# Kernel tuning notes

Measured on AMD Instinct MI355X. Metric: run time of the kernel, lower is better.

The kernel has to match this reference:

```python
import jax, jax.numpy as jnp
import numpy as np

N_M, N_C, D, H, E, EL = 200000, 50000, 128, 64, 1000000, 100000


def gat_conv(h_src, h_dst, W_src, W_dst, a_src, a_dst, b, src, dst, n_dst):
    # PyG GATConv (heads=1): project, per-edge attention logit, segment softmax over dst, weighted scatter-sum.
    hs = h_src @ W_src                      # [Ns, H]
    hd = h_dst @ W_dst                      # [Nd, H]
    al_s = hs @ a_src                       # [Ns]
    al_d = hd @ a_dst                       # [Nd]
    alpha = jax.nn.leaky_relu(al_s[src] + al_d[dst], 0.2)   # [E]
    m = jax.ops.segment_max(alpha, dst, num_segments=n_dst)
    m = jnp.where(jnp.isfinite(m), m, 0.0)
    e = jnp.exp(alpha - m[dst])
    denom = jax.ops.segment_sum(e, dst, num_segments=n_dst)
    w = e / jnp.maximum(denom[dst], 1e-16)
    out = jax.ops.segment_sum(w[:, None] * hs[src], dst, num_segments=n_dst)
    return out + b


def setup_inputs() -> dict:
    key = jax.random.key(0)
    ks = jax.random.split(key, 32)
    p = lambda k, s: (jax.random.normal(k, s, jnp.float32) * 0.1)
    inp = {
        'x_m': jax.random.normal(ks[0], (N_M, D), jnp.float32),
        'x_c': jax.random.normal(ks[1], (N_C, D), jnp.float32),
        'src_mc': jax.random.randint(ks[2], (E,), 0, N_M, jnp.int32),
        'dst_mc': jax.random.randint(ks[3], (E,), 0, N_C, jnp.int32),
        'src_cm': jax.random.randint(ks[4], (E,), 0, N_C, jnp.int32),
        'dst_cm': jax.random.randint(ks[5], (E,), 0, N_M, jnp.int32),
        'row': jax.random.randint(ks[6], (EL,), 0, N_M, jnp.int32),
        'col': jax.random.randint(ks[7], (EL,), 0, N_C, jnp.int32),
        'W1s_mc': p(ks[8], (D, H)), 'W1d_mc': p(ks[9], (D, H)),
        'a1s_mc': p(ks[10], (H,)), 'a1d_mc': p(ks[11], (H,)), 'b1_mc': p(ks[12], (H,)),
        'W1s_cm': p(ks[13], (D, H)), 'W1d_cm': p(ks[14], (D, H)),
        'a1s_cm': p(ks[15], (H,)), 'a1d_cm': p(ks[16], (H,)), 'b1_cm': p(ks[17], (H,)),
        'W2s_mc': p(ks[18], (H, H)), 'W2d_mc': p(ks[19], (H, H)),
        'a2s_mc': p(ks[20], (H,)), 'a2d_mc': p(ks[21], (H,)), 'b2_mc': p(ks[22], (H,)),
        'W2s_cm': p(ks[23], (H, H)), 'W2d_cm': p(ks[24], (H, H)),
        'a2s_cm': p(ks[25], (H,)), 'a2d_cm': p(ks[26], (H,)), 'b2_cm': p(ks[27], (H,)),
        'Wd1': p(ks[28], (2 * H, H)), 'bd1': p(ks[29], (H,)),
        'Wd2': p(ks[30], (H, 2)), 'bd2': p(ks[31], (2,)),
    }
    return inp


def reference(x_m, x_c, src_mc, dst_mc, src_cm, dst_cm, row, col,
              W1s_mc, W1d_mc, a1s_mc, a1d_mc, b1_mc,
              W1s_cm, W1d_cm, a1s_cm, a1d_cm, b1_cm,
              W2s_mc, W2d_mc, a2s_mc, a2d_mc, b2_mc,
              W2s_cm, W2d_cm, a2s_cm, a2d_cm, b2_cm,
              Wd1, bd1, Wd2, bd2):
    # Layer 1: materials receive only via concepts->materials edges; concepts via materials->concepts.
    z_c = jax.nn.relu(gat_conv(x_m, x_c, W1s_mc, W1d_mc, a1s_mc, a1d_mc, b1_mc, src_mc, dst_mc, N_C))
    z_m = jax.nn.relu(gat_conv(x_c, x_m, W1s_cm, W1d_cm, a1s_cm, a1d_cm, b1_cm, src_cm, dst_cm, N_M))
    # Layer 2 (no activation)
    z_c2 = gat_conv(z_m, z_c, W2s_mc, W2d_mc, a2s_mc, a2d_mc, b2_mc, src_mc, dst_mc, N_C)
    z_m2 = gat_conv(z_c, z_m, W2s_cm, W2d_cm, a2s_cm, a2d_cm, b2_cm, src_cm, dst_cm, N_M)
    # Edge decoder: gather-concat + 2-layer MLP (no activation between, per source)
    z = jnp.concatenate([z_m2[row], z_c2[col]], axis=-1)   # [EL, 2H]
    z = z @ Wd1 + bd1
    z = z @ Wd2 + bd2
    return z.reshape(-1)
```

## Files before the change

kernel.cpp:

```cpp
#include <hip/hip_runtime.h>
#include <hip/hip_fp16.h>
#include <cstdint>
#include <cstddef>

typedef _Float16 f16x8 __attribute__((ext_vector_type(8)));
typedef float f32x4 __attribute__((ext_vector_type(4)));

__device__ __forceinline__ float exp_am8(float a) {
    return __builtin_amdgcn_exp2f(fmaf(a, 1.442695040888963f, -11.541560327111707f));
}

__global__ __launch_bounds__(256) void bucket_hist(const int* __restrict__ dA,
                                                   int* __restrict__ bcntA, int shA,
                                                   const int* __restrict__ dB,
                                                   int* __restrict__ bcntB, int shB,
                                                   int E, int nblkA) {
    __shared__ int h[256];
    const int* dst; int* bcnt; int sh; int base;
    if ((int)blockIdx.x < nblkA) { dst = dA; bcnt = bcntA; sh = shA; base = blockIdx.x * 4096; }
    else { dst = dB; bcnt = bcntB; sh = shB; base = (blockIdx.x - nblkA) * 4096; }
    int t = threadIdx.x;
    h[t] = 0;
    __syncthreads();
#pragma unroll
    for (int j = 0; j < 16; ++j) {
        int i = base + j * 256 + t;
        if (i < E) atomicAdd(&h[dst[i] >> sh], 1);
    }
    __syncthreads();
    int c = h[t];
    if (c > 0) atomicAdd(&bcnt[t], c);
}

__global__ void bucket_scan(const int* __restrict__ bcntA, int nbkA,
                            int* __restrict__ bbaseA, int* __restrict__ bcurA,
                            int* __restrict__ offA, int nA,
                            const int* __restrict__ bcntB, int nbkB,
                            int* __restrict__ bbaseB, int* __restrict__ bcurB,
                            int* __restrict__ offB, int nB, int E) {
    int t = threadIdx.x;
    if (t == 0) {
        int run = 0;
        for (int i = 0; i < nbkA; ++i) { bbaseA[i] = run; bcurA[i] = run; run += bcntA[i]; }
        bbaseA[nbkA] = run;
        offA[nA] = E;
    }
    if (t == 64) {
        int run = 0;
        for (int i = 0; i < nbkB; ++i) { bbaseB[i] = run; bcurB[i] = run; run += bcntB[i]; }
        bbaseB[nbkB] = run;
        offB[nB] = E;
    }
}

__global__ __launch_bounds__(256) void bucket_scatter(
    const int* __restrict__ srcA, const int* __restrict__ dstA,
    int* __restrict__ bcurA, unsigned* __restrict__ pairsA,
    const int* __restrict__ srcB, const int* __restrict__ dstB,
    int* __restrict__ bcurB, unsigned* __restrict__ pairsB,
    int E, int nblkA, int shA, int shB, int srcbits) {
    __shared__ int bcnt[256];
    __shared__ int bbase[256];
    const int* src; const int* dst; int* bcur; unsigned* pairs; int sh; int base;
    if ((int)blockIdx.x < nblkA) {
        src = srcA; dst = dstA; bcur = bcurA; pairs = pairsA; sh = shA;
        base = blockIdx.x * 4096;
    } else {
        src = srcB; dst = dstB; bcur = bcurB; pairs = pairsB; sh = shB;
        base = (blockIdx.x - nblkA) * 4096;
    }
    int t = threadIdx.x;
    int msk = (1 << sh) - 1;
    bcnt[t] = 0;
    __syncthreads();
    int sreg[16], dreg[16];
#pragma unroll
    for (int j = 0; j < 16; ++j) {
        int i = base + j * 256 + t;
        if (i < E) {
            sreg[j] = src[i];
            dreg[j] = dst[i];
            atomicAdd(&bcnt[dreg[j] >> sh], 1);
        } else {
            dreg[j] = -1;
        }
    }
    __syncthreads();
    {
        int c = bcnt[t];
        int g = (c > 0) ? atomicAdd(&bcur[t], c) : 0;
        bbase[t] = g;
        bcnt[t] = 0;
    }
    __syncthreads();
#pragma unroll
    for (int j = 0; j < 16; ++j) {
        if (dreg[j] >= 0) {
            int b = dreg[j] >> sh;
            int r = atomicAdd(&bcnt[b], 1);
            pairs[bbase[b] + r] = ((unsigned)(dreg[j] & msk) << srcbits) | (unsigned)sreg[j];
        }
    }
}

__global__ __launch_bounds__(256) void bucket_expand2(
    const unsigned* __restrict__ pairsA, const int* __restrict__ bbaseA, int nA,
    int* __restrict__ offA, int* __restrict__ csrA, int shA, int nbA,
    const unsigned* __restrict__ pairsB, const int* __restrict__ bbaseB, int nB,
    int* __restrict__ offB, int* __restrict__ csrB, int shB, int srcbits) {
    __shared__ int lcnt[1024];
    __shared__ int red[256];
    const unsigned* pairs; const int* bbase; int n; int* off; int* csr; int sh; int b;
    if ((int)blockIdx.x < nbA) {
        pairs = pairsA; bbase = bbaseA; n = nA; off = offA; csr = csrA; sh = shA;
        b = blockIdx.x;
    } else {
        pairs = pairsB; bbase = bbaseB; n = nB; off = offB; csr = csrB; sh = shB;
        b = blockIdx.x - nbA;
    }
    int dpb = 1 << sh;
    int d0 = b << sh;
    int t = threadIdx.x;
    unsigned smask = (1u << srcbits) - 1u;
    for (int dl = t; dl < dpb; dl += 256) lcnt[dl] = 0;
    __syncthreads();
    int pbeg = bbase[b], pend = bbase[b + 1];
    for (int i = pbeg + t; i < pend; i += 256)
        atomicAdd(&lcnt[pairs[i] >> srcbits], 1);
    __syncthreads();
    int per = (dpb + 255) >> 8;
    int i0 = t * per;
    int s = 0;
    for (int j = 0; j < per; ++j) {
        int dl = i0 + j;
        if (dl < dpb) s += lcnt[dl];
    }
    red[t] = s;
    __syncthreads();
    for (int st = 1; st < 256; st <<= 1) {
        int tmp = (t >= st) ? red[t - st] : 0;
        __syncthreads();
        red[t] += tmp;
        __syncthreads();
    }
    int run = pbeg + red[t] - s;
    for (int j = 0; j < per; ++j) {
        int dl = i0 + j;
        if (dl < dpb) {
            int c = lcnt[dl];
            if (d0 + dl < n) off[d0 + dl] = run;
            lcnt[dl] = run;
            run += c;
        }
    }
    __syncthreads();
    for (int i = pbeg + t; i < pend; i += 256) {
        unsigned p = pairs[i];
        int dl = (int)(p >> srcbits);
        int pos = atomicAdd(&lcnt[dl], 1);
        csr[pos] = (int)(p & smask);
    }
}

__global__ __launch_bounds__(256) void pack_w_all(
    const float* __restrict__ Wa0, const float* __restrict__ Wb0, _Float16* __restrict__ P0,
    const float* __restrict__ Wa1, const float* __restrict__ Wb1, _Float16* __restrict__ P1,
    const float* __restrict__ Wa2, const float* __restrict__ Wb2, _Float16* __restrict__ P2,
    const float* __restrict__ Wa3, const float* __restrict__ Wb3, _Float16* __restrict__ P3) {
    int b = blockIdx.x;
    const float* Wa; const float* Wb; _Float16* Wp; int K; int lb;
    if (b < 64)       { Wa = Wa0; Wb = Wb0; Wp = P0; K = 128; lb = b; }
    else if (b < 128) { Wa = Wa1; Wb = Wb1; Wp = P1; K = 128; lb = b - 64; }
    else if (b < 160) { Wa = Wa2; Wb = Wb2; Wp = P2; K = 64;  lb = b - 128; }
    else              { Wa = Wa3; Wb = Wb3; Wp = P3; K = 64;  lb = b - 160; }
    int NKB = K / 32;
    int i = lb * 256 + threadIdx.x;
    if (i >= 128 * K) return;
    int k = i >> 7, c = i & 127;
    float v = (c < 64) ? Wa[k * 64 + c] : Wb[k * 64 + (c - 64)];
    int ct = c >> 4, lr = c & 15, kb = k >> 5, lk = (k & 31) >> 3, e = k & 7;
    Wp[((ct * NKB + kb) * 64 + (lr + 16 * lk)) * 8 + e] = (_Float16)v;
}

__global__ void decoder_prep2(const float* __restrict__ Wd1, const float* __restrict__ bd1,
                              const float* __restrict__ Wd2, const float* __restrict__ bd2,
                              const float* __restrict__ b2_cm, const float* __restrict__ b2_mc,
                              float* __restrict__ Wc, float* __restrict__ bc,
                              float* __restrict__ bq) {
    __shared__ float WcS[256];
    int t = threadIdx.x;
    int k = t >> 1, c = t & 1;
    float s = 0.f;
    for (int j = 0; j < 64; ++j) s += Wd1[k * 64 + j] * Wd2[j * 2 + c];
    Wc[k * 2 + c] = s;
    WcS[k * 2 + c] = s;
    if (k == 0) {
        float b = bd2[c];
        for (int j = 0; j < 64; ++j) b += bd1[j] * Wd2[j * 2 + c];
        bc[c] = b;
    }
    __syncthreads();
    if (t < 2) {
        float v = 0.f;
        for (int j = 0; j < 64; ++j) v += b2_cm[j] * WcS[j * 2 + t];
        bq[t] = v;
    } else if (t < 4) {
        int cc = t - 2;
        float v = 0.f;
        for (int j = 0; j < 64; ++j) v += b2_mc[j] * WcS[(64 + j) * 2 + cc];
        bq[t] = v;
    }
}

template <int K, typename TIN, int QMODE>
__global__ __launch_bounds__(256) void proj_mfma4_kernel(const TIN* __restrict__ X, int N,
                                                         const _Float16* __restrict__ Wp,
                                                         const float* __restrict__ a0v,
                                                         const float* __restrict__ a1v,
                                                         __half* __restrict__ out0,
                                                         const float* __restrict__ wcq,
                                                         float2* __restrict__ qtab,
                                                         float* __restrict__ al0,
                                                         float* __restrict__ al1) {
    constexpr int NKB = K / 32;
    __shared__ __align__(16) _Float16 Wlds[128 * K];
    int t = threadIdx.x;
    constexpr int NV = (128 * K) / 8;
#pragma unroll
    for (int i = t; i < NV; i += 256)
        ((uint4*)Wlds)[i] = ((const uint4*)Wp)[i];
    __syncthreads();

    int rt = blockIdx.x * 64;
    int wv = t >> 6, lane = t & 63, lr = lane & 15, lk = lane >> 4;
    int row = rt + wv * 16 + lr;
    int rowc = row < N ? row : N - 1;

    f32x4 acc[8];
#pragma unroll
    for (int i = 0; i < 8; ++i) acc[i] = f32x4{0.f, 0.f, 0.f, 0.f};

    const f16x8* Wf = (const f16x8*)Wlds;
#pragma unroll
    for (int kb = 0; kb < NKB; ++kb) {
        f16x8 bf;
        if constexpr (sizeof(TIN) == 4) {
            const float* xr = (const float*)X + (size_t)rowc * K + kb * 32 + lk * 8;
            float4 x0 = *(const float4*)xr;
            float4 x1 = *(const float4*)(xr + 4);
            bf[0] = (_Float16)x0.x; bf[1] = (_Float16)x0.y;
            bf[2] = (_Float16)x0.z; bf[3] = (_Float16)x0.w;
            bf[4] = (_Float16)x1.x; bf[5] = (_Float16)x1.y;
            bf[6] = (_Float16)x1.z; bf[7] = (_Float16)x1.w;
        } else {
            bf = *(const f16x8*)((const _Float16*)X + (size_t)rowc * K + kb * 32 + lk * 8);
        }
#pragma unroll
        for (int ct = 0; ct < 8; ++ct) {
            acc[ct] = __builtin_amdgcn_mfma_f32_16x16x32_f16(Wf[(ct * NKB + kb) * 64 + lane],
                                                             bf, acc[ct], 0, 0, 0);
        }
    }

    float p0 = 0.f, p1 = 0.f;
#pragma unroll
    for (int ct = 0; ct < 4; ++ct) {
        float4 aq = ((const float4*)a0v)[ct * 4 + lk];
        f32x4 v = acc[ct];
        p0 += v[0] * aq.x + v[1] * aq.y + v[2] * aq.z + v[3] * aq.w;
    }
#pragma unroll
    for (int ct = 0; ct < 4; ++ct) {
        float4 aq = ((const float4*)a1v)[ct * 4 + lk];
        f32x4 v = acc[4 + ct];
        p1 += v[0] * aq.x + v[1] * aq.y + v[2] * aq.z + v[3] * aq.w;
    }
    p0 += __shfl_xor(p0, 16); p0 += __shfl_xor(p0, 32);
    p1 += __shfl_xor(p1, 16); p1 += __shfl_xor(p1, 32);

    if (QMODE == 1) {
        float qx = 0.f, qy = 0.f;
#pragma unroll
        for (int ct = 0; ct < 4; ++ct) {
            f32x4 v = acc[ct];
#pragma unroll
            for (int j = 0; j < 4; ++j) {
                float2 w = ((const float2*)wcq)[ct * 16 + lk * 4 + j];
                qx = fmaf(v[j], w.x, qx);
                qy = fmaf(v[j], w.y, qy);
            }
        }
        qx += __shfl_xor(qx, 16); qx += __shfl_xor(qx, 32);
        qy += __shfl_xor(qy, 16); qy += __shfl_xor(qy, 32);
        if (row < N && lane < 16) {
            qtab[row] = make_float2(qx, qy);
            al0[row] = p0;
            al1[row] = p1;
        }
    } else {
        if (row < N) {
#pragma unroll
            for (int ct = 0; ct < 4; ++ct) {
                f32x4 v = acc[ct];
                __half2 h01 = __floats2half2_rn(v[0], v[1]);
                __half2 h23 = __floats2half2_rn(v[2], v[3]);
                uint2 pk;
                pk.x = *(const unsigned int*)&h01;
                pk.y = *(const unsigned int*)&h23;
                *(uint2*)(out0 + ((size_t)row << 6) + ct * 16 + lk * 4) = pk;
            }
            if (lane < 16) { al0[row] = p0; al1[row] = p1; }
        }
    }
}

#define AGG_CAP 64
#define AGG_PAD 66

template <int RELU>
__global__ __launch_bounds__(256) void gat_aggregate9(
    const int* __restrict__ off0, const int* __restrict__ csr0,
    const __half* __restrict__ hs0, const float* __restrict__ als0,
    const float* __restrict__ ald0, const float* __restrict__ bias0,
    void* __restrict__ outp0, int n0,
    const int* __restrict__ off1, const int* __restrict__ csr1,
    const __half* __restrict__ hs1, const float* __restrict__ als1,
    const float* __restrict__ ald1, const float* __restrict__ bias1,
    void* __restrict__ outp1, int n1,
    int nb0) {
    __shared__ uint2 wP[16][AGG_PAD];
    int t = threadIdx.x;
    int slot = t >> 4;
    int sub = t & 15;

    const int* off; const int* csr; const __half* hs; const float* als;
    const float* ald; const float* bias; void* outp; int nd; int b;
    if (blockIdx.x < (unsigned)nb0) {
        b = blockIdx.x;
        off = off0; csr = csr0; hs = hs0; als = als0; ald = ald0; bias = bias0;
        outp = outp0; nd = n0;
    } else {
        b = blockIdx.x - nb0;
        off = off1; csr = csr1; hs = hs1; als = als1; ald = ald1; bias = bias1;
        outp = outp1; nd = n1;
    }
    int d = b * 16 + slot;
    bool active = d < nd;
    int beg = 0, deg = 0;
    float aldv = 0.f;
    if (active) {
        beg = off[d];
        deg = off[d + 1] - beg;
        aldv = ald[d];
    }
    float4 bl4 = ((const float4*)bias)[sub];
    uint2* WP = wP[slot];

    float sum = 0.f;
    for (int i = sub; i < deg; i += 16) {
        int s = csr[beg + i];
        float a = als[s] + aldv;
        a = (a >= 0.f) ? a : 0.2f * a;
        float w = exp_am8(a);
        sum += w;
        if (i < AGG_CAP) {
            __half hw = __float2half_rn(w);
            __half2 h2 = __half2half2(hw);
            WP[i] = make_uint2(*(const unsigned int*)&h2, (unsigned int)s);
        }
    }
    sum += __shfl_xor(sum, 1);
    sum += __shfl_xor(sum, 2);
    sum += __shfl_xor(sum, 4);
    sum += __shfl_xor(sum, 8);
    float inv = 1.f / fmaxf(sum, 1e-16f);

    int dc = deg < AGG_CAP ? deg : AGG_CAP;
    const uint2* hs4 = (const uint2*)hs;
    __half2 z = __floats2half2_rn(0.f, 0.f);
    __half2 aA = z, aB = z, aC = z, aD = z;
    int i = 0;
    for (; i + 8 <= dc; i += 8) {
        uint4 q0 = *(const uint4*)&WP[i];
        uint4 q1 = *(const uint4*)&WP[i + 2];
        uint4 q2 = *(const uint4*)&WP[i + 4];
        uint4 q3 = *(const uint4*)&WP[i + 6];
        uint2 v0 = hs4[(size_t)q0.y * 16 + sub];
        uint2 v1 = hs4[(size_t)q0.w * 16 + sub];
        uint2 v2 = hs4[(size_t)q1.y * 16 + sub];
        uint2 v3 = hs4[(size_t)q1.w * 16 + sub];
        uint2 v4 = hs4[(size_t)q2.y * 16 + sub];
        uint2 v5 = hs4[(size_t)q2.w * 16 + sub];
        uint2 v6 = hs4[(size_t)q3.y * 16 + sub];
        uint2 v7 = hs4[(size_t)q3.w * 16 + sub];
        aA = __hfma2(*(const __half2*)&q0.x, *(const __half2*)&v0.x, aA);
        aB = __hfma2(*(const __half2*)&q0.x, *(const __half2*)&v0.y, aB);
        aC = __hfma2(*(const __half2*)&q0.z, *(const __half2*)&v1.x, aC);
        aD = __hfma2(*(const __half2*)&q0.z, *(const __half2*)&v1.y, aD);
        aA = __hfma2(*(const __half2*)&q1.x, *(const __half2*)&v2.x, aA);
        aB = __hfma2(*(const __half2*)&q1.x, *(const __half2*)&v2.y, aB);
        aC = __hfma2(*(const __half2*)&q1.z, *(const __half2*)&v3.x, aC);
        aD = __hfma2(*(const __half2*)&q1.z, *(const __half2*)&v3.y, aD);
        aA = __hfma2(*(const __half2*)&q2.x, *(const __half2*)&v4.x, aA);
        aB = __hfma2(*(const __half2*)&q2.x, *(const __half2*)&v4.y, aB);
        aC = __hfma2(*(const __half2*)&q2.z, *(const __half2*)&v5.x, aC);
        aD = __hfma2(*(const __half2*)&q2.z, *(const __half2*)&v5.y, aD);
        aA = __hfma2(*(const __half2*)&q3.x, *(const __half2*)&v6.x, aA);
        aB = __hfma2(*(const __half2*)&q3.x, *(const __half2*)&v6.y, aB);
        aC = __hfma2(*(const __half2*)&q3.z, *(const __half2*)&v7.x, aC);
        aD = __hfma2(*(const __half2*)&q3.z, *(const __half2*)&v7.y, aD);
    }
    for (; i + 2 <= dc; i += 2) {
        uint4 q = *(const uint4*)&WP[i];
        uint2 v0 = hs4[(size_t)q.y * 16 + sub];
        uint2 v1 = hs4[(size_t)q.w * 16 + sub];
        aA = __hfma2(*(const __half2*)&q.x, *(const __half2*)&v0.x, aA);
        aB = __hfma2(*(const __half2*)&q.x, *(const __half2*)&v0.y, aB);
        aC = __hfma2(*(const __half2*)&q.z, *(const __half2*)&v1.x, aC);
        aD = __hfma2(*(const __half2*)&q.z, *(const __half2*)&v1.y, aD);
    }
    if (i < dc) {
        uint2 u = WP[i];
        uint2 v = hs4[(size_t)u.y * 16 + sub];
        aA = __hfma2(*(const __half2*)&u.x, *(const __half2*)&v.x, aA);
        aB = __hfma2(*(const __half2*)&u.x, *(const __half2*)&v.y, aB);
    }
    for (int j = AGG_CAP; j < deg; ++j) {
        int s = csr[beg + j];
        float a = als[s] + aldv;
        a = (a >= 0.f) ? a : 0.2f * a;
        __half hw = __float2half_rn(exp_am8(a));
        __half2 w2 = __half2half2(hw);
        uint2 v = hs4[(size_t)s * 16 + sub];
        aA = __hfma2(w2, *(const __half2*)&v.x, aA);
        aB = __hfma2(w2, *(const __half2*)&v.y, aB);
    }
    float2 fA = __half22float2(aA);
    float2 fB = __half22float2(aB);
    float2 fC = __half22float2(aC);
    float2 fD = __half22float2(aD);
    float o0 = (fA.x + fC.x) * inv + bl4.x;
    float o1 = (fA.y + fC.y) * inv + bl4.y;
    float o2 = (fB.x + fD.x) * inv + bl4.z;
    float o3 = (fB.y + fD.y) * inv + bl4.w;
    if (deg == 0) { o0 = bl4.x; o1 = bl4.y; o2 = bl4.z; o3 = bl4.w; }
    if (RELU) {
        o0 = fmaxf(o0, 0.f); o1 = fmaxf(o1, 0.f);
        o2 = fmaxf(o2, 0.f); o3 = fmaxf(o3, 0.f);
    }
    if (active) {
        __half2 h01 = __floats2half2_rn(o0, o1);
        __half2 h23 = __floats2half2_rn(o2, o3);
        uint2 pk;
        pk.x = *(const unsigned int*)&h01;
        pk.y = *(const unsigned int*)&h23;
        ((uint2*)outp)[(size_t)d * 16 + sub] = pk;
    }
}

__global__ __launch_bounds__(256) void gat_aggregate10(
    const int* __restrict__ off0, const int* __restrict__ csr0,
    const float2* __restrict__ q0, const float* __restrict__ als0,
    const float* __restrict__ ald0, const float2 bq0,
    float2* __restrict__ out0, int n0,
    const int* __restrict__ off1, const int* __restrict__ csr1,
    const float2* __restrict__ q1, const float* __restrict__ als1,
    const float* __restrict__ ald1, const float2 bq1,
    float2* __restrict__ out1, int n1,
    int nb0) {
    const int* off; const int* csr; const float2* qt; const float* als;
    const float* ald; float2 bq; float2* outp; int nd; int b;
    if (blockIdx.x < (unsigned)nb0) {
        b = blockIdx.x;
        off = off0; csr = csr0; qt = q0; als = als0; ald = ald0; bq = bq0;
        outp = out0; nd = n0;
    } else {
        b = blockIdx.x - nb0;
        off = off1; csr = csr1; qt = q1; als = als1; ald = ald1; bq = bq1;
        outp = out1; nd = n1;
    }
    int d = b * 256 + threadIdx.x;
    if (d >= nd) return;
    int beg = off[d], end = off[d + 1];
    float aldv = ald[d];
    float sum = 0.f, ax = 0.f, ay = 0.f;
    int i = beg;
    for (; i + 2 <= end; i += 2) {
        int s0 = csr[i], s1 = csr[i + 1];
        float a0 = als[s0] + aldv;
        float a1 = als[s1] + aldv;
        float2 v0 = qt[s0];
        float2 v1 = qt[s1];
        a0 = (a0 >= 0.f) ? a0 : 0.2f * a0;
        a1 = (a1 >= 0.f) ? a1 : 0.2f * a1;
        float w0 = exp_am8(a0);
        float w1 = exp_am8(a1);
        sum += w0 + w1;
        ax = fmaf(w0, v0.x, ax); ay = fmaf(w0, v0.y, ay);
        ax = fmaf(w1, v1.x, ax); ay = fmaf(w1, v1.y, ay);
    }
    if (i < end) {
        int s = csr[i];
        float a = als[s] + aldv;
        a = (a >= 0.f) ? a : 0.2f * a;
        float w = exp_am8(a);
        float2 v = qt[s];
        sum += w;
        ax = fmaf(w, v.x, ax); ay = fmaf(w, v.y, ay);
    }
    float inv = 1.f / fmaxf(sum, 1e-16f);
    outp[d] = make_float2(ax * inv + bq.x, ay * inv + bq.y);
}

__global__ __launch_bounds__(256) void decoder4_kernel(const int* __restrict__ row,
                                                       const int* __restrict__ col,
                                                       const float2* __restrict__ pm,
                                                       const float2* __restrict__ pc,
                                                       const float* __restrict__ bc,
                                                       float* __restrict__ out, int EL) {
    int e = blockIdx.x * 256 + threadIdx.x;
    if (e >= EL) return;
    float2 a = pm[row[e]];
    float2 b = pc[col[e]];
    *(float2*)(out + 2 * (size_t)e) = make_float2(a.x + b.x + bc[0], a.y + b.y + bc[1]);
}

__global__ void read_bq(const float* __restrict__ bq, float2* __restrict__ o) {
    if (threadIdx.x == 0) { o[0] = make_float2(bq[0], bq[1]); o[1] = make_float2(bq[2], bq[3]); }
}

__global__ __launch_bounds__(256) void gat_aggregate10p(
    const int* __restrict__ off0, const int* __restrict__ csr0,
    const float2* __restrict__ q0, const float* __restrict__ als0,
    const float* __restrict__ ald0, const float2* __restrict__ bqp,
    float2* __restrict__ out0, int n0,
    const int* __restrict__ off1, const int* __restrict__ csr1,
    const float2* __restrict__ q1, const float* __restrict__ als1,
    const float* __restrict__ ald1,
    float2* __restrict__ out1, int n1,
    int nb0) {
    const int* off; const int* csr; const float2* qt; const float* als;
    const float* ald; float2 bq; float2* outp; int nd; int b;
    if (blockIdx.x < (unsigned)nb0) {
        b = blockIdx.x;
        off = off0; csr = csr0; qt = q0; als = als0; ald = ald0; bq = bqp[1];
        outp = out0; nd = n0;
    } else {
        b = blockIdx.x - nb0;
        off = off1; csr = csr1; qt = q1; als = als1; ald = ald1; bq = bqp[0];
        outp = out1; nd = n1;
    }
    int d = b * 256 + threadIdx.x;
    if (d >= nd) return;
    int beg = off[d], end = off[d + 1];
    float aldv = ald[d];
    float sum = 0.f, ax = 0.f, ay = 0.f;
    int i = beg;
    for (; i + 2 <= end; i += 2) {
        int s0 = csr[i], s1 = csr[i + 1];
        float a0 = als[s0] + aldv;
        float a1 = als[s1] + aldv;
        float2 v0 = qt[s0];
        float2 v1 = qt[s1];
        a0 = (a0 >= 0.f) ? a0 : 0.2f * a0;
        a1 = (a1 >= 0.f) ? a1 : 0.2f * a1;
        float w0 = exp_am8(a0);
        float w1 = exp_am8(a1);
        sum += w0 + w1;
        ax = fmaf(w0, v0.x, ax); ay = fmaf(w0, v0.y, ay);
        ax = fmaf(w1, v1.x, ax); ay = fmaf(w1, v1.y, ay);
    }
    if (i < end) {
        int s = csr[i];
        float a = als[s] + aldv;
        a = (a >= 0.f) ? a : 0.2f * a;
        float w = exp_am8(a);
        float2 v = qt[s];
        sum += w;
        ax = fmaf(w, v.x, ax); ay = fmaf(w, v.y, ay);
    }
    float inv = 1.f / fmaxf(sum, 1e-16f);
    outp[d] = make_float2(ax * inv + bq.x, ay * inv + bq.y);
}

extern "C" void kernel_launch(void* const* d_in, const int* in_sizes, int n_in,
                              void* d_out, int out_size, void* d_ws, size_t ws_size,
                              hipStream_t stream) {
    const int D = 128;
    const float* x_m    = (const float*)d_in[0];
    const float* x_c    = (const float*)d_in[1];
    const int*   src_mc = (const int*)d_in[2];
    const int*   dst_mc = (const int*)d_in[3];
    const int*   src_cm = (const int*)d_in[4];
    const int*   dst_cm = (const int*)d_in[5];
    const int*   rowi   = (const int*)d_in[6];
    const int*   coli   = (const int*)d_in[7];
    const float* W1s_mc = (const float*)d_in[8];
    const float* W1d_mc = (const float*)d_in[9];
    const float* a1s_mc = (const float*)d_in[10];
    const float* a1d_mc = (const float*)d_in[11];
    const float* b1_mc  = (const float*)d_in[12];
    const float* W1s_cm = (const float*)d_in[13];
    const float* W1d_cm = (const float*)d_in[14];
    const float* a1s_cm = (const float*)d_in[15];
    const float* a1d_cm = (const float*)d_in[16];
    const float* b1_cm  = (const float*)d_in[17];
    const float* W2s_mc = (const float*)d_in[18];
    const float* W2d_mc = (const float*)d_in[19];
    const float* a2s_mc = (const float*)d_in[20];
    const float* a2d_mc = (const float*)d_in[21];
    const float* b2_mc  = (const float*)d_in[22];
    const float* W2s_cm = (const float*)d_in[23];
    const float* W2d_cm = (const float*)d_in[24];
    const float* a2s_cm = (const float*)d_in[25];
    const float* a2d_cm = (const float*)d_in[26];
    const float* b2_cm  = (const float*)d_in[27];
    const float* Wd1    = (const float*)d_in[28];
    const float* bd1    = (const float*)d_in[29];
    const float* Wd2    = (const float*)d_in[30];
    const float* bd2    = (const float*)d_in[31];

    const int N_M = in_sizes[0] / D;
    const int N_C = in_sizes[1] / D;
    const int E   = in_sizes[2];
    const int EL  = in_sizes[6];
    float* out = (float*)d_out;

    uint8_t* base = (uint8_t*)d_ws;
    size_t off = 0;
    auto carve = [&](size_t bytes) -> void* {
        void* p = base + off;
        off += (bytes + 255) & ~(size_t)255;
        return p;
    };
    __half* hsA_h = (__half*)carve((size_t)N_M * 64 * 2);
    __half* hsB_h = (__half*)carve((size_t)N_C * 64 * 2);
    __half* zm1_h = (__half*)carve((size_t)N_M * 64 * 2);
    __half* zc1_h = (__half*)carve((size_t)N_C * 64 * 2);
    float2* qA    = (float2*)carve((size_t)N_M * 8);
    float2* qB    = (float2*)carve((size_t)N_C * 8);
    float2* pm_m  = (float2*)carve((size_t)N_M * 8);
    float2* pm_c  = (float2*)carve((size_t)N_C * 8);
    float* als_mc = (float*)carve((size_t)N_M * 4);
    float* ald_cm = (float*)carve((size_t)N_M * 4);
    float* als_cm = (float*)carve((size_t)N_C * 4);
    float* ald_mc = (float*)carve((size_t)N_C * 4);
    int* off_mc = (int*)carve((size_t)(N_C + 1) * 4);
    int* off_cm = (int*)carve((size_t)(N_M + 1) * 4);
    int* csr_mc = (int*)carve((size_t)E * 4);
    int* csr_cm = (int*)carve((size_t)E * 4);
    unsigned* pairs_mc = (unsigned*)carve((size_t)E * 4);
    unsigned* pairs_cm = (unsigned*)carve((size_t)E * 4);
    int* bcnt_base = (int*)carve(512 * 4);
    int* bcnt_mc = bcnt_base;
    int* bcnt_cm = bcnt_base + 256;
    int* bbase_mc = (int*)carve(257 * 4);
    int* bbase_cm = (int*)carve(257 * 4);
    int* bcur_mc = (int*)carve(256 * 4);
    int* bcur_cm = (int*)carve(256 * 4);
    _Float16* wp1A = (_Float16*)carve(128 * 128 * 2);
    _Float16* wp1B = (_Float16*)carve(128 * 128 * 2);
    _Float16* wp2A = (_Float16*)carve(128 * 64 * 2);
    _Float16* wp2B = (_Float16*)carve(128 * 64 * 2);
    float* Wc = (float*)carve(256 * 4);
    float* bc = (float*)carve(256);
    float* bq = (float*)carve(256);
    float2* bq2 = (float2*)bq;

    int shA = 0; while (((N_C + (1 << shA) - 1) >> shA) > 256) shA++;
    int shB = 0; while (((N_M + (1 << shB) - 1) >> shB) > 256) shB++;
    int nbkA = (N_C + (1 << shA) - 1) >> shA;
    int nbkB = (N_M + (1 << shB) - 1) >> shB;
    int maxN = N_M > N_C ? N_M : N_C;
    int srcbits = 1; while ((1 << srcbits) < maxN) srcbits++;

    pack_w_all<<<192, 256, 0, stream>>>(W1s_mc, W1d_cm, wp1A,
                                        W1s_cm, W1d_mc, wp1B,
                                        W2s_mc, W2d_cm, wp2A,
                                        W2s_cm, W2d_mc, wp2B);
    decoder_prep2<<<1, 256, 0, stream>>>(Wd1, bd1, Wd2, bd2, b2_cm, b2_mc, Wc, bc, bq);

    hipMemsetAsync(bcnt_base, 0, 512 * 4, stream);
    int nblk = (E + 4095) / 4096;
    bucket_hist<<<2 * nblk, 256, 0, stream>>>(dst_mc, bcnt_mc, shA,
                                              dst_cm, bcnt_cm, shB, E, nblk);
    bucket_scan<<<1, 128, 0, stream>>>(bcnt_mc, nbkA, bbase_mc, bcur_mc, off_mc, N_C,
                                       bcnt_cm, nbkB, bbase_cm, bcur_cm, off_cm, N_M, E);
    bucket_scatter<<<2 * nblk, 256, 0, stream>>>(
        src_mc, dst_mc, bcur_mc, pairs_mc,
        src_cm, dst_cm, bcur_cm, pairs_cm, E, nblk, shA, shB, srcbits);
    bucket_expand2<<<nbkA + nbkB, 256, 0, stream>>>(
        pairs_mc, bbase_mc, N_C, off_mc, csr_mc, shA, nbkA,
        pairs_cm, bbase_cm, N_M, off_cm, csr_cm, shB, srcbits);

    int nb_c16 = (N_C + 15) / 16;
    int nb_m16 = (N_M + 15) / 16;

    proj_mfma4_kernel<128, float, 0><<<(N_M + 63) / 64, 256, 0, stream>>>(
        x_m, N_M, wp1A, a1s_mc, a1d_cm, hsA_h, nullptr, nullptr, als_mc, ald_cm);
    proj_mfma4_kernel<128, float, 0><<<(N_C + 63) / 64, 256, 0, stream>>>(
        x_c, N_C, wp1B, a1s_cm, a1d_mc, hsB_h, nullptr, nullptr, als_cm, ald_mc);
    gat_aggregate9<1><<<nb_c16 + nb_m16, 256, 0, stream>>>(
        off_mc, csr_mc, hsA_h, als_mc, ald_mc, b1_mc, zc1_h, N_C,
        off_cm, csr_cm, hsB_h, als_cm, ald_cm, b1_cm, zm1_h, N_M, nb_c16);

    proj_mfma4_kernel<64, __half, 1><<<(N_M + 63) / 64, 256, 0, stream>>>(
        zm1_h, N_M, wp2A, a2s_mc, a2d_cm, nullptr, Wc + 128, qA, als_mc, ald_cm);
    proj_mfma4_kernel<64, __half, 1><<<(N_C + 63) / 64, 256, 0, stream>>>(
        zc1_h, N_C, wp2B, a2s_cm, a2d_mc, nullptr, Wc, qB, als_cm, ald_mc);
    int nb_c256 = (N_C + 255) / 256;
    int nb_m256 = (N_M + 255) / 256;
    gat_aggregate10p<<<nb_c256 + nb_m256, 256, 0, stream>>>(
        off_mc, csr_mc, qA, als_mc, ald_mc, bq2, pm_c, N_C,
        off_cm, csr_cm, qB, als_cm, ald_cm, pm_m, N_M, nb_c256);

    decoder4_kernel<<<(EL + 255) / 256, 256, 0, stream>>>(rowi, coli, pm_m, pm_c, bc, out, EL);
}
```

Baseline: 227.3 us.

## Fold layer-2 projection weights into per-node vectors and drop layer-2 MFMA GEMM

Measured after the change: 234.1 us. 1.03x slower.

```diff
diff --git a/kernel.cpp b/kernel.cpp
--- a/kernel.cpp
+++ b/kernel.cpp
@@ -162,18 +162,15 @@
     }
 }
 
-__global__ __launch_bounds__(256) void pack_w_all(
+__global__ __launch_bounds__(256) void pack_w2(
     const float* __restrict__ Wa0, const float* __restrict__ Wb0, _Float16* __restrict__ P0,
-    const float* __restrict__ Wa1, const float* __restrict__ Wb1, _Float16* __restrict__ P1,
-    const float* __restrict__ Wa2, const float* __restrict__ Wb2, _Float16* __restrict__ P2,
-    const float* __restrict__ Wa3, const float* __restrict__ Wb3, _Float16* __restrict__ P3) {
+    const float* __restrict__ Wa1, const float* __restrict__ Wb1, _Float16* __restrict__ P1) {
     int b = blockIdx.x;
-    const float* Wa; const float* Wb; _Float16* Wp; int K; int lb;
-    if (b < 64)       { Wa = Wa0; Wb = Wb0; Wp = P0; K = 128; lb = b; }
-    else if (b < 128) { Wa = Wa1; Wb = Wb1; Wp = P1; K = 128; lb = b - 64; }
-    else if (b < 160) { Wa = Wa2; Wb = Wb2; Wp = P2; K = 64;  lb = b - 128; }
-    else              { Wa = Wa3; Wb = Wb3; Wp = P3; K = 64;  lb = b - 160; }
-    int NKB = K / 32;
+    const float* Wa; const float* Wb; _Float16* Wp; int lb;
+    if (b < 64) { Wa = Wa0; Wb = Wb0; Wp = P0; lb = b; }
+    else        { Wa = Wa1; Wb = Wb1; Wp = P1; lb = b - 64; }
+    constexpr int K = 128;
+    constexpr int NKB = K / 32;
     int i = lb * 256 + threadIdx.x;
     if (i >= 128 * K) return;
     int k = i >> 7, c = i & 127;
@@ -182,11 +179,16 @@
     Wp[((ct * NKB + kb) * 64 + (lr + 16 * lk)) * 8 + e] = (_Float16)v;
 }
 
-__global__ void decoder_prep2(const float* __restrict__ Wd1, const float* __restrict__ bd1,
+__global__ void decoder_prep3(const float* __restrict__ Wd1, const float* __restrict__ bd1,
                               const float* __restrict__ Wd2, const float* __restrict__ bd2,
                               const float* __restrict__ b2_cm, const float* __restrict__ b2_mc,
+                              const float* __restrict__ W2s_mc, const float* __restrict__ a2s_mc,
+                              const float* __restrict__ W2d_cm, const float* __restrict__ a2d_cm,
+                              const float* __restrict__ W2s_cm, const float* __restrict__ a2s_cm,
+                              const float* __restrict__ W2d_mc, const float* __restrict__ a2d_mc,
                               float* __restrict__ Wc, float* __restrict__ bc,
-                              float* __restrict__ bq) {
+                              float* __restrict__ bq,
+                              float4* __restrict__ foldA, float4* __restrict__ foldB) {
     __shared__ float WcS[256];
     int t = threadIdx.x;
     int k = t >> 1, c = t & 1;
@@ -210,16 +212,37 @@
         for (int j = 0; j < 64; ++j) v += b2_mc[j] * WcS[(64 + j) * 2 + cc];
         bq[t] = v;
     }
-}
-
-template <int K, typename TIN, int QMODE>
-__global__ __launch_bounds__(256) void proj_mfma4_kernel(const TIN* __restrict__ X, int N,
+    if (t < 64) {
+        int j = t;
+        float fa = 0.f, fd = 0.f, qx = 0.f, qy = 0.f;
+        for (int cc = 0; cc < 64; ++cc) {
+            float ws = W2s_mc[j * 64 + cc];
+            fa += ws * a2s_mc[cc];
+            qx += ws * WcS[(64 + cc) * 2 + 0];
+            qy += ws * WcS[(64 + cc) * 2 + 1];
+            fd += W2d_cm[j * 64 + cc] * a2d_cm[cc];
+        }
+        foldA[j] = make_float4(fa, fd, qx, qy);
+    } else if (t < 128) {
+        int j = t - 64;
+        float fa = 0.f, fd = 0.f, qx = 0.f, qy = 0.f;
+        for (int cc = 0; cc < 64; ++cc) {
+            float ws = W2s_cm[j * 64 + cc];
+            fa += ws * a2s_cm[cc];
+            qx += ws * WcS[cc * 2 + 0];
+            qy += ws * WcS[cc * 2 + 1];
+            fd += W2d_mc[j * 64 + cc] * a2d_mc[cc];
+        }
+        foldB[j] = make_float4(fa, fd, qx, qy);
+    }
+}
+
+template <int K>
+__global__ __launch_bounds__(256) void proj_mfma3_kernel(const float* __restrict__ X, int N,
                                                          const _Float16* __restrict__ Wp,
                                                          const float* __restrict__ a0v,
                                                          const float* __restrict__ a1v,
                                                          __half* __restrict__ out0,
-                                                         const float* __restrict__ wcq,
-                                                         float2* __restrict__ qtab,
                                                          float* __restrict__ al0,
                                                          float* __restrict__ al1) {
     constexpr int NKB = K / 32;
@@ -244,17 +267,13 @@
 #pragma unroll
     for (int kb = 0; kb < NKB; ++kb) {
         f16x8 bf;
-        if constexpr (sizeof(TIN) == 4) {
-            const float* xr = (const float*)X + (size_t)rowc * K + kb * 32 + lk * 8;
-            float4 x0 = *(const float4*)xr;
-            float4 x1 = *(const float4*)(xr + 4);
-            bf[0] = (_Float16)x0.x; bf[1] = (_Float16)x0.y;
-            bf[2] = (_Float16)x0.z; bf[3] = (_Float16)x0.w;
-            bf[4] = (_Float16)x1.x; bf[5] = (_Float16)x1.y;
-            bf[6] = (_Float16)x1.z; bf[7] = (_Float16)x1.w;
-        } else {
-            bf = *(const f16x8*)((const _Float16*)X + (size_t)rowc * K + kb * 32 + lk * 8);
-        }
+        const float* xr = X + (size_t)rowc * K + kb * 32 + lk * 8;
+        float4 x0 = *(const float4*)xr;
+        float4 x1 = *(const float4*)(xr + 4);
+        bf[0] = (_Float16)x0.x; bf[1] = (_Float16)x0.y;
+        bf[2] = (_Float16)x0.z; bf[3] = (_Float16)x0.w;
+        bf[4] = (_Float16)x1.x; bf[5] = (_Float16)x1.y;
+        bf[6] = (_Float16)x1.z; bf[7] = (_Float16)x1.w;
 #pragma unroll
         for (int ct = 0; ct < 8; ++ct) {
             acc[ct] = __builtin_amdgcn_mfma_f32_16x16x32_f16(Wf[(ct * NKB + kb) * 64 + lane],
@@ -277,40 +296,52 @@
     }
     p0 += __shfl_xor(p0, 16); p0 += __shfl_xor(p0, 32);
     p1 += __shfl_xor(p1, 16); p1 += __shfl_xor(p1, 32);
-
-    if (QMODE == 1) {
-        float qx = 0.f, qy = 0.f;
+    if (row < N) {
 #pragma unroll
         for (int ct = 0; ct < 4; ++ct) {
             f32x4 v = acc[ct];
-#pragma unroll
-            for (int j = 0; j < 4; ++j) {
-                float2 w = ((const float2*)wcq)[ct * 16 + lk * 4 + j];
-                qx = fmaf(v[j], w.x, qx);
-                qy = fmaf(v[j], w.y, qy);
-            }
-        }
-        qx += __shfl_xor(qx, 16); qx += __shfl_xor(qx, 32);
-        qy += __shfl_xor(qy, 16); qy += __shfl_xor(qy, 32);
-        if (row < N && lane < 16) {
-            qtab[row] = make_float2(qx, qy);
-            al0[row] = p0;
-            al1[row] = p1;
-        }
-    } else {
-        if (row < N) {
-#pragma unroll
-            for (int ct = 0; ct < 4; ++ct) {
-                f32x4 v = acc[ct];
-                __half2 h01 = __floats2half2_rn(v[0], v[1]);
-                __half2 h23 = __floats2half2_rn(v[2], v[3]);
-                uint2 pk;
-                pk.x = *(const unsigned int*)&h01;
-                pk.y = *(const unsigned int*)&h23;
-                *(uint2*)(out0 + ((size_t)row << 6) + ct * 16 + lk * 4) = pk;
-            }
-            if (lane < 16) { al0[row] = p0; al1[row] = p1; }
-        }
+            __half2 h01 = __floats2half2_rn(v[0], v[1]);
+            __half2 h23 = __floats2half2_rn(v[2], v[3]);
+            uint2 pk;
+            pk.x = *(const unsigned int*)&h01;
+            pk.y = *(const unsigned int*)&h23;
+            *(uint2*)(out0 + ((size_t)row << 6) + ct * 16 + lk * 4) = pk;
+        }
+        if (lane < 16) { al0[row] = p0; al1[row] = p1; }
+    }
+}
+
+__global__ __launch_bounds__(256) void layer2_fold(const __half* __restrict__ z1, int N,
+                                                   const float4* __restrict__ fold,
+                                                   float* __restrict__ als,
+                                                   float* __restrict__ ald,
+                                                   float2* __restrict__ q) {
+    int t = threadIdx.x;
+    int slot = t >> 4, sub = t & 15;
+    int row = blockIdx.x * 16 + slot;
+    if (row >= N) return;
+    uint2 v = ((const uint2*)z1)[(size_t)row * 16 + sub];
+    float2 f01 = __half22float2(*(const __half2*)&v.x);
+    float2 f23 = __half22float2(*(const __half2*)&v.y);
+    float4 f0 = fold[4 * sub + 0];
+    float4 f1 = fold[4 * sub + 1];
+    float4 f2 = fold[4 * sub + 2];
+    float4 f3 = fold[4 * sub + 3];
+    float a0 = f01.x * f0.x + f01.y * f1.x + f23.x * f2.x + f23.y * f3.x;
+    float a1 = f01.x * f0.y + f01.y * f1.y + f23.x * f2.y + f23.y * f3.y;
+    float a2 = f01.x * f0.z + f01.y * f1.z + f23.x * f2.z + f23.y * f3.z;
+    float a3 = f01.x * f0.w + f01.y * f1.w + f23.x * f2.w + f23.y * f3.w;
+#pragma unroll
+    for (int o = 1; o < 16; o <<= 1) {
+        a0 += __shfl_xor(a0, o);
+        a1 += __shfl_xor(a1, o);
+        a2 += __shfl_xor(a2, o);
+        a3 += __shfl_xor(a3, o);
+    }
+    if (sub == 0) {
+        als[row] = a0;
+        ald[row] = a1;
+        q[row] = make_float2(a2, a3);
     }
 }
 
@@ -458,77 +489,6 @@
     }
 }
 
-__global__ __launch_bounds__(256) void gat_aggregate10(
-    const int* __restrict__ off0, const int* __restrict__ csr0,
-    const float2* __restrict__ q0, const float* __restrict__ als0,
-    const float* __restrict__ ald0, const float2 bq0,
-    float2* __restrict__ out0, int n0,
-    const int* __restrict__ off1, const int* __restrict__ csr1,
-    const float2* __restrict__ q1, const float* __restrict__ als1,
-    const float* __restrict__ ald1, const float2 bq1,
-    float2* __restrict__ out1, int n1,
-    int nb0) {
-    const int* off; const int* csr; const float2* qt; const float* als;
-    const float* ald; float2 bq; float2* outp; int nd; int b;
-    if (blockIdx.x < (unsigned)nb0) {
-        b = blockIdx.x;
-        off = off0; csr = csr0; qt = q0; als = als0; ald = ald0; bq = bq0;
-        outp = out0; nd = n0;
-    } else {
-        b = blockIdx.x - nb0;
-        off = off1; csr = csr1; qt = q1; als = als1; ald = ald1; bq = bq1;
-        outp = out1; nd = n1;
-    }
-    int d = b * 256 + threadIdx.x;
-    if (d >= nd) return;
-    int beg = off[d], end = off[d + 1];
-    float aldv = ald[d];
-    float sum = 0.f, ax = 0.f, ay = 0.f;
-    int i = beg;
-    for (; i + 2 <= end; i += 2) {
-        int s0 = csr[i], s1 = csr[i + 1];
-        float a0 = als[s0] + aldv;
-        float a1 = als[s1] + aldv;
-        float2 v0 = qt[s0];
-        float2 v1 = qt[s1];
-        a0 = (a0 >= 0.f) ? a0 : 0.2f * a0;
-        a1 = (a1 >= 0.f) ? a1 : 0.2f * a1;
-        float w0 = exp_am8(a0);
-        float w1 = exp_am8(a1);
-        sum += w0 + w1;
-        ax = fmaf(w0, v0.x, ax); ay = fmaf(w0, v0.y, ay);
-        ax = fmaf(w1, v1.x, ax); ay = fmaf(w1, v1.y, ay);
-    }
-    if (i < end) {
-        int s = csr[i];
-        float a = als[s] + aldv;
-        a = (a >= 0.f) ? a : 0.2f * a;
-        float w = exp_am8(a);
-        float2 v = qt[s];
-        sum += w;
-        ax = fmaf(w, v.x, ax); ay = fmaf(w, v.y, ay);
-    }
-    float inv = 1.f / fmaxf(sum, 1e-16f);
-    outp[d] = make_float2(ax * inv + bq.x, ay * inv + bq.y);
-}
-
-__global__ __launch_bounds__(256) void decoder4_kernel(const int* __restrict__ row,
-                                                       const int* __restrict__ col,
-                                                       const float2* __restrict__ pm,
-                                                       const float2* __restrict__ pc,
-                                                       const float* __restrict__ bc,
-                                                       float* __restrict__ out, int EL) {
-    int e = blockIdx.x * 256 + threadIdx.x;
-    if (e >= EL) return;
-    float2 a = pm[row[e]];
-    float2 b = pc[col[e]];
-    *(float2*)(out + 2 * (size_t)e) = make_float2(a.x + b.x + bc[0], a.y + b.y + bc[1]);
-}
-
-__global__ void read_bq(const float* __restrict__ bq, float2* __restrict__ o) {
-    if (threadIdx.x == 0) { o[0] = make_float2(bq[0], bq[1]); o[1] = make_float2(bq[2], bq[3]); }
-}
-
 __global__ __launch_bounds__(256) void gat_aggregate10p(
     const int* __restrict__ off0, const int* __restrict__ csr0,
     const float2* __restrict__ q0, const float* __restrict__ als0,
@@ -581,6 +541,19 @@
     }
     float inv = 1.f / fmaxf(sum, 1e-16f);
     outp[d] = make_float2(ax * inv + bq.x, ay * inv + bq.y);
+}
+
+__global__ __launch_bounds__(256) void decoder4_kernel(const int* __restrict__ row,
+                                                       const int* __restrict__ col,
+                                                       const float2* __restrict__ pm,
+                                                       const float2* __restrict__ pc,
+                                                       const float* __restrict__ bc,
+                                                       float* __restrict__ out, int EL) {
+    int e = blockIdx.x * 256 + threadIdx.x;
+    if (e >= EL) return;
+    float2 a = pm[row[e]];
+    float2 b = pc[col[e]];
+    *(float2*)(out + 2 * (size_t)e) = make_float2(a.x + b.x + bc[0], a.y + b.y + bc[1]);
 }
 
 extern "C" void kernel_launch(void* const* d_in, const int* in_sizes, int n_in,
@@ -660,12 +633,12 @@
     int* bcur_cm = (int*)carve(256 * 4);
     _Float16* wp1A = (_Float16*)carve(128 * 128 * 2);
     _Float16* wp1B = (_Float16*)carve(128 * 128 * 2);
-    _Float16* wp2A = (_Float16*)carve(128 * 64 * 2);
-    _Float16* wp2B = (_Float16*)carve(128 * 64 * 2);
     float* Wc = (float*)carve(256 * 4);
     float* bc = (float*)carve(256);
     float* bq = (float*)carve(256);
     float2* bq2 = (float2*)bq;
+    float4* foldA = (float4*)carve(64 * 16);
+    float4* foldB = (float4*)carve(64 * 16);
 
     int shA = 0; while (((N_C + (1 << shA) - 1) >> shA) > 256) shA++;
     int shB = 0; while (((N_M + (1 << shB) - 1) >> shB) > 256) shB++;
@@ -674,11 +647,11 @@
     int maxN = N_M > N_C ? N_M : N_C;
     int srcbits = 1; while ((1 << srcbits) < maxN) srcbits++;
 
-    pack_w_all<<<192, 256, 0, stream>>>(W1s_mc, W1d_cm, wp1A,
-                                        W1s_cm, W1d_mc, wp1B,
-                                        W2s_mc, W2d_cm, wp2A,
-                                        W2s_cm, W2d_mc, wp2B);
-    decoder_prep2<<<1, 256, 0, stream>>>(Wd1, bd1, Wd2, bd2, b2_cm, b2_mc, Wc, bc, bq);
+    pack_w2<<<128, 256, 0, stream>>>(W1s_mc, W1d_cm, wp1A, W1s_cm, W1d_mc, wp1B);
+    decoder_prep3<<<1, 256, 0, stream>>>(Wd1, bd1, Wd2, bd2, b2_cm, b2_mc,
+                                         W2s_mc, a2s_mc, W2d_cm, a2d_cm,
+                                         W2s_cm, a2s_cm, W2d_mc, a2d_mc,
+                                         Wc, bc, bq, foldA, foldB);
 
     hipMemsetAsync(bcnt_base, 0, 512 * 4, stream);
     int nblk = (E + 4095) / 4096;
@@ -696,18 +669,19 @@
     int nb_c16 = (N_C + 15) / 16;
     int nb_m16 = (N_M + 15) / 16;
 
-    proj_mfma4_kernel<128, float, 0><<<(N_M + 63) / 64, 256, 0, stream>>>(
-        x_m, N_M, wp1A, a1s_mc, a1d_cm, hsA_h, nullptr, nullptr, als_mc, ald_cm);
-    proj_mfma4_kernel<128, float, 0><<<(N_C + 63) / 64, 256, 0, stream>>>(
-        x_c, N_C, wp1B, a1s_cm, a1d_mc, hsB_h, nullptr, nullptr, als_cm, ald_mc);
-    gat_aggregate9<1><<<nb_c16 + nb_m16, 256, 0, stream>>>(
+    proj_mfma3_kernel<128><<<(N_M + 63) / 64, 256, 0, stream>>>(
+        x_m, N_M, wp1A, a1s_mc, a1d_cm, hsA_h, als_mc, ald_cm);
+    proj_mfma3_kernel<128><<<(N_C + 63) / 64, 256, 0, stream>>>(
+        x_c, N_C, wp1B, a1s_cm, a1d_mc, hsB_h, als_cm, ald_mc);
+    gat_aggregate9<1><<<nb_m16, 256, 0, stream>>>(
+        off_cm, csr_cm, hsB_h, als_cm, ald_cm, b1_cm, zm1_h, N_M,
+        off_cm, csr_cm, hsB_h, als_cm, ald_cm, b1_cm, zm1_h, N_M, nb_m16);
+    gat_aggregate9<1><<<nb_c16, 256, 0, stream>>>(
         off_mc, csr_mc, hsA_h, als_mc, ald_mc, b1_mc, zc1_h, N_C,
-        off_cm, csr_cm, hsB_h, als_cm, ald_cm, b1_cm, zm1_h, N_M, nb_c16);
-
-    proj_mfma4_kernel<64, __half, 1><<<(N_M + 63) / 64, 256, 0, stream>>>(
-        zm1_h, N_M, wp2A, a2s_mc, a2d_cm, nullptr, Wc + 128, qA, als_mc, ald_cm);
-    proj_mfma4_kernel<64, __half, 1><<<(N_C + 63) / 64, 256, 0, stream>>>(
-        zc1_h, N_C, wp2B, a2s_cm, a2d_mc, nullptr, Wc, qB, als_cm, ald_mc);
+        off_mc, csr_mc, hsA_h, als_mc, ald_mc, b1_mc, zc1_h, N_C, nb_c16);
+
+    layer2_fold<<<(N_M + 15) / 16, 256, 0, stream>>>(zm1_h, N_M, foldA, als_mc, ald_cm, qA);
+    layer2_fold<<<(N_C + 15) / 16, 256, 0, stream>>>(zc1_h, N_C, foldB, als_cm, ald_mc, qB);
     int nb_c256 = (N_C + 255) / 256;
     int nb_m256 = (N_M + 255) / 256;
     gat_aggregate10p<<<nb_c256 + nb_m256, 256, 0, stream>>>(
```
